# Kernel tuning notes

Measured on AMD Instinct MI355X. Metric: run time of the kernel, lower is better.

The kernel has to match this reference:

```python
import math
import jax, jax.numpy as jnp
import numpy as np

B, C_IN, C_OUT, K, STYLE, H, W = 16, 512, 512, 3, 512, 64, 64


def setup_inputs() -> dict:
    key = jax.random.key(0)
    k1, k2, k3, k4 = jax.random.split(key, 4)
    return {
        "x": jax.random.normal(k1, (B, C_IN, H, W), jnp.float32),
        "style": jax.random.normal(k2, (B, STYLE), jnp.float32),
        "weight": jax.random.normal(k3, (C_OUT, C_IN, K, K), jnp.float32),  # learned conv weight (leading 1 dim of torch param squeezed)
        "mod_w": jax.random.normal(k4, (C_IN, STYLE), jnp.float32),         # EqualLinear weight
        "mod_b": jnp.ones((C_IN,), jnp.float32),                             # EqualLinear bias (bias_init=1)
    }


def reference(x, style, weight, mod_w, mod_b):
    # EqualLinear modulation: scale = 1/sqrt(style_dim), lr_mul = 1
    mod_scale = 1.0 / math.sqrt(STYLE)
    s = style @ (mod_w.T * mod_scale) + mod_b            # [B, C_IN]

    # per-sample modulated weight
    w_scale = 1.0 / math.sqrt(C_IN * K * K)
    w = w_scale * weight[None] * s[:, None, :, None, None]  # [B, C_OUT, C_IN, K, K]

    # demodulate
    demod = jax.lax.rsqrt(jnp.sum(w * w, axis=(2, 3, 4)) + 1e-8)  # [B, C_OUT]
    w = w * demod[:, :, None, None, None]

    pad = K // 2

    def conv_one(xi, wi):
        # xi: [C_IN, H, W], wi: [C_OUT, C_IN, K, K]
        return jax.lax.conv_general_dilated(
            xi[None], wi, window_strides=(1, 1),
            padding=[(pad, pad), (pad, pad)],
            dimension_numbers=("NCHW", "OIHW", "NCHW"),
        )[0]

    return jax.vmap(conv_one)(x, w)  # [B, C_OUT, H, W]
```

## Files before the change

### kernel.cpp

```cpp
#include <hip/hip_runtime.h>
#include <hip/hip_bf16.h>
#include <math.h>
#include <stdint.h>

#define B_     16
#define CI_    512
#define CO_    512
#define HH     64
#define WW     64
#define STYLE_ 512

typedef __bf16 bf16x8 __attribute__((ext_vector_type(8)));
typedef float f32x16 __attribute__((ext_vector_type(16)));

__device__ __forceinline__ int fsl(int r, int h) {
    return (2 * r + (h ^ ((r >> 2) & 1))) ^ (((r >> 4) & 1) << 1);
}

#define WS_S     0
#define WS_DEMOD 32768
#define WS_WSQ   65536
#define WS_WB    1114112
#define WS_XS    5832704

__device__ __forceinline__ void gload16(const void* g, void* l) {
    __builtin_amdgcn_global_load_lds((const __attribute__((address_space(1))) uint32_t*)g,
                                     (__attribute__((address_space(3))) uint32_t*)l, 16, 0, 0);
}

__global__ __launch_bounds__(256) void k_style2(const float* __restrict__ style,
                                                const float* __restrict__ mod_w,
                                                const float* __restrict__ mod_b,
                                                float* __restrict__ s_out) {
    const int ci   = blockIdx.x * 4 + (threadIdx.x >> 6);
    const int b    = blockIdx.y;
    const int lane = threadIdx.x & 63;
    const float4* mw = (const float4*)(mod_w + (size_t)ci * STYLE_);
    const float4* st = (const float4*)(style + (size_t)b * STYLE_);
    float acc = 0.f;
    #pragma unroll
    for (int i = 0; i < 2; ++i) {
        float4 a = mw[lane + i * 64], s = st[lane + i * 64];
        acc += a.x * s.x + a.y * s.y + a.z * s.z + a.w * s.w;
    }
    #pragma unroll
    for (int off = 32; off >= 1; off >>= 1) acc += __shfl_xor(acc, off);
    if (lane == 0)
        s_out[b * CI_ + ci] = acc * 0.044194173824159216f + mod_b[ci];
}

__global__ __launch_bounds__(256) void k_wprep(const float* __restrict__ weight,
                                               float* __restrict__ wsq, __bf16* __restrict__ wb) {
    int p = blockIdx.x * 256 + threadIdx.x;
    int co = p >> 9, ci = p & 511;
    const float* wp = weight + (size_t)p * 9;
    const int sl = fsl(co & 127, (ci >> 3) & 1);
    const int gs = ((co >> 7) << 8) + sl;
    float acc = 0.f;
    #pragma unroll
    for (int t = 0; t < 9; ++t) {
        float v = wp[t];
        acc += v * v;
        wb[(((size_t)(ci >> 4) * 9 + t) * 8192) + gs * 8 + (ci & 7)] = (__bf16)v;
    }
    wsq[(size_t)ci * CO_ + co] = acc;
}

__global__ void k_demod(const float* __restrict__ s, const float* __restrict__ wsq,
                        float* __restrict__ demod) {
    int b = blockIdx.x, co = threadIdx.x;
    const float w_scale2 = 1.0f / 4608.0f;
    float acc = 0.f;
    const float* sb = s + b * CI_;
    for (int ci = 0; ci < CI_; ++ci) { float sv = sb[ci]; acc += sv * sv * wsq[(size_t)ci * CO_ + co]; }
    demod[b * CO_ + co] = 1.0f / sqrtf(acc * w_scale2 + 1e-8f);
}

__global__ __launch_bounds__(256) void k_xs(const float* __restrict__ x, const float* __restrict__ s,
                                            __bf16* __restrict__ xs) {
    __shared__ float Lt[64][65];
    const int y = blockIdx.x, b = blockIdx.y;
    const int tid = threadIdx.x;
    const float w_scale = 0.014731391274719739f;
    for (int ci0 = 0; ci0 < CI_; ci0 += 64) {
        for (int i = tid; i < 64 * 16; i += 256) {
            int ci = i >> 4, x4 = (i & 15) * 4;
            const float4 v = *(const float4*)&x[((size_t)(b * CI_ + ci0 + ci) * HH + y) * WW + x4];
            float sc = s[b * CI_ + ci0 + ci] * w_scale;
            Lt[ci][x4]     = v.x * sc;
            Lt[ci][x4 + 1] = v.y * sc;
            Lt[ci][x4 + 2] = v.z * sc;
            Lt[ci][x4 + 3] = v.w * sc;
        }
        __syncthreads();
        for (int o = tid; o < 512; o += 256) {
            int xx = o >> 3, oct = o & 7;
            int cb = ci0 + oct * 8;
            int chunk = cb >> 4;
            int pp = fsl(xx + 1, oct & 1) - 2;
            bf16x8 v;
            #pragma unroll
            for (int j = 0; j < 8; ++j) v[j] = (__bf16)Lt[oct * 8 + j][xx];
            size_t idx = (((size_t)chunk * 16 + b) * 66 + (y + 1)) * 1024 + pp * 8;
            *(bf16x8*)&xs[idx] = v;
        }
        __syncthreads();
    }
    if (y == 0 || y == 63) {
        const int row = (y == 0) ? 0 : 65;
        uint32_t* xs32 = (uint32_t*)xs;
        for (int c = 0; c < 32; ++c)
            for (int i = tid; i < 512; i += 256)
                xs32[(((size_t)c * 16 + b) * 66 + row) * 512 + i] = 0;
    }
}

#define XBUF 25600
#define WBUF 36864

__global__ __launch_bounds__(512, 1) void k_conv(
    const __bf16* __restrict__ xs, const __bf16* __restrict__ wb,
    const float* __restrict__ demod, float* __restrict__ out)
{
    __shared__ __align__(512) char smem[2 * XBUF + 2 * WBUF];

    const int tid  = threadIdx.x;
    const int lane = tid & 63;
    const int wave = tid >> 6;

    const int bid  = blockIdx.x;
    const int r8   = bid & 7;
    const int q    = bid >> 3;
    const int co0  = (q & 3) * 128;
    const int yb   = (q >> 2) | (r8 << 4);
    const int y0   = (yb & 7) * 8;
    const int b    = yb >> 3;

    const int lm = lane & 31;
    const int g2 = lane >> 5;

    if (tid < 320) {
        int buf = tid / 160, rem = tid % 160;
        int rb = rem >> 4, hh = rem & 15;
        int side = hh >> 3, dw = hh & 7;
        ((uint32_t*)smem)[buf * (XBUF / 4) + rb * 640 + side * 520 + dw] = 0;
    }
    asm volatile("s_waitcnt lgkmcnt(0)" ::: "memory");

    uint32_t soff[9];
    uint32_t sdst[9];
    if (wave < 4) {
        #pragma unroll
        for (int i = 0; i < 5; ++i) {
            int j = wave * 5 + i, rb = j >> 1, seg = j & 1;
            soff[i] = (uint32_t)((y0 + rb) * 1024 + seg * 512 + lane * 8);
            sdst[i] = (uint32_t)(rb * 2560 + 32 + seg * 1024 + lane * 16);
        }
    } else {
        #pragma unroll
        for (int i = 0; i < 9; ++i) {
            int j = (wave - 4) * 9 + i;
            int tap = j >> 2, seg = j & 3;
            soff[i] = (uint32_t)(tap * 8192 + co0 * 16 + seg * 512 + lane * 8);
            sdst[i] = (uint32_t)(j * 1024 + lane * 16);
        }
    }

    const uint32_t abase = (uint32_t)(16 * fsl(lm, g2));
    uint32_t bbase[9];
    #pragma unroll
    for (int kh = 0; kh < 3; ++kh)
        #pragma unroll
        for (int kw = 0; kw < 3; ++kw)
            bbase[kh * 3 + kw] = (uint32_t)((wave + kh) * 2560 + 16 * fsl(lm + kw, g2));

    f32x16 acc[4][2];
    #pragma unroll
    for (int mi = 0; mi < 4; ++mi)
        #pragma unroll
        for (int nt = 0; nt < 2; ++nt)
            #pragma unroll
            for (int r = 0; r < 16; ++r) acc[mi][nt][r] = 0.f;

    auto stage = [&](int chunk, int sel) {
        if (wave < 4) {
            const __bf16* base = xs + (size_t)chunk * 1081344 + (size_t)b * 67584;
            #pragma unroll
            for (int i = 0; i < 5; ++i) gload16(base + soff[i], smem + sel * XBUF + sdst[i]);
        } else {
            const __bf16* base = wb + (size_t)chunk * 73728;
            #pragma unroll
            for (int i = 0; i < 9; ++i) gload16(base + soff[i], smem + 2 * XBUF + sel * WBUF + sdst[i]);
        }
    };

    stage(0, 0);

    for (int t = 0; t < 32; ++t) {
        if (t < 31) {
            stage(t + 1, (t + 1) & 1);
            if (wave < 4) asm volatile("s_waitcnt vmcnt(5)" ::: "memory");
            else          asm volatile("s_waitcnt vmcnt(9)" ::: "memory");
        } else {
            asm volatile("s_waitcnt vmcnt(0)" ::: "memory");
        }
        __builtin_amdgcn_s_barrier();

        const char* xbuf = smem + (t & 1) * XBUF;
        const char* wbuf = smem + 2 * XBUF + (t & 1) * WBUF + abase;

        bf16x8 fa[2][4];
        bf16x8 fb[2][2];
        #pragma unroll
        for (int mi = 0; mi < 4; ++mi) fa[0][mi] = *(const bf16x8*)(wbuf + mi * 1024);
        #pragma unroll
        for (int nt = 0; nt < 2; ++nt) fb[0][nt] = *(const bf16x8*)(xbuf + bbase[0] + nt * 1024);

        __builtin_amdgcn_s_setprio(1);
        #pragma unroll
        for (int tp = 0; tp < 9; ++tp) {
            const int cur = tp & 1, nxt = cur ^ 1;
            if (tp < 8) {
                const char* wp = wbuf + (tp + 1) * 4096;
                #pragma unroll
                for (int mi = 0; mi < 4; ++mi) fa[nxt][mi] = *(const bf16x8*)(wp + mi * 1024);
                #pragma unroll
                for (int nt = 0; nt < 2; ++nt) fb[nxt][nt] = *(const bf16x8*)(xbuf + bbase[tp + 1] + nt * 1024);
            }
            __builtin_amdgcn_sched_barrier(0);
            #pragma unroll
            for (int nt = 0; nt < 2; ++nt) {
                acc[0][nt] = __builtin_amdgcn_mfma_f32_32x32x16_bf16(fa[cur][0], fb[cur][nt], acc[0][nt], 0, 0, 0);
                acc[1][nt] = __builtin_amdgcn_mfma_f32_32x32x16_bf16(fa[cur][1], fb[cur][nt], acc[1][nt], 0, 0, 0);
                acc[2][nt] = __builtin_amdgcn_mfma_f32_32x32x16_bf16(fa[cur][2], fb[cur][nt], acc[2][nt], 0, 0, 0);
                acc[3][nt] = __builtin_amdgcn_mfma_f32_32x32x16_bf16(fa[cur][3], fb[cur][nt], acc[3][nt], 0, 0, 0);
            }
            __builtin_amdgcn_sched_barrier(0);
        }
        __builtin_amdgcn_s_setprio(0);
        __builtin_amdgcn_s_barrier();
    }

    const int y = y0 + wave;
    float* outb = out + (size_t)b * CO_ * 4096 + (size_t)y * 64;
    #pragma unroll
    for (int mi = 0; mi < 4; ++mi) {
        #pragma unroll
        for (int reg = 0; reg < 16; ++reg) {
            const int co = co0 + mi * 32 + (reg & 3) + 8 * (reg >> 2) + 4 * g2;
            const float dm = demod[b * CO_ + co];
            outb[(size_t)co * 4096 + lm]      = acc[mi][0][reg] * dm;
            outb[(size_t)co * 4096 + 32 + lm] = acc[mi][1][reg] * dm;
        }
    }
}

extern "C" void kernel_launch(void* const* d_in, const int* in_sizes, int n_in,
                              void* d_out, int out_size, void* d_ws, size_t ws_size,
                              hipStream_t stream) {
    const float* x      = (const float*)d_in[0];
    const float* style  = (const float*)d_in[1];
    const float* weight = (const float*)d_in[2];
    const float* mod_w  = (const float*)d_in[3];
    const float* mod_b  = (const float*)d_in[4];
    float* out = (float*)d_out;

    char* wsb = (char*)d_ws;
    float*  s_buf = (float*)(wsb + WS_S);
    float*  demod = (float*)(wsb + WS_DEMOD);
    float*  wsq   = (float*)(wsb + WS_WSQ);
    __bf16* wb    = (__bf16*)(wsb + WS_WB);
    __bf16* xs    = (__bf16*)(wsb + WS_XS);

    k_style2<<<dim3(CI_ / 4, B_), dim3(256), 0, stream>>>(style, mod_w, mod_b, s_buf);
    k_wprep<<<dim3(CO_ * CI_ / 256), dim3(256), 0, stream>>>(weight, wsq, wb);
    k_demod<<<dim3(B_), dim3(CO_), 0, stream>>>(s_buf, wsq, demod);
    k_xs<<<dim3(HH, B_), dim3(256), 0, stream>>>(x, s_buf, xs);
    k_conv<<<dim3(512), dim3(512), 0, stream>>>(xs, wb, demod, out);
}
```

Measured before the change: 328.7 us.

## Retile conv to 64-channel blocks with 4 waves and cross-row input reuse

The conv kernel is retiled from 128 output channels x 8 rows per 512-thread block to 64 output channels x 8 rows per 256-thread block, with two blocks per CU and 1024 blocks in total. Each wave now computes two output rows and reuses the loaded input rows across the three kh taps. It loads 4 input-row fragments per kw instead of reloading per tap, which cuts LDS reads per MFMA. The weight prep layout and the LDS row stride change to match. The cost is more global weight traffic per output, because each block covers fewer channels, and the software pipelining of fragment loads across taps is dropped.

New measurement: 319.7 us. -2.7%, faster.

```diff
diff --git a/kernel.cpp b/kernel.cpp
--- a/kernel.cpp
+++ b/kernel.cpp
@@ -54,8 +54,7 @@
     int p = blockIdx.x * 256 + threadIdx.x;
     int co = p >> 9, ci = p & 511;
     const float* wp = weight + (size_t)p * 9;
-    const int sl = fsl(co & 127, (ci >> 3) & 1);
-    const int gs = ((co >> 7) << 8) + sl;
+    const int gs = ((co >> 6) << 7) + fsl(co & 63, (ci >> 3) & 1);
     float acc = 0.f;
     #pragma unroll
     for (int t = 0; t < 9; ++t) {
@@ -115,14 +114,14 @@
     }
 }
 
-#define XBUF 25600
-#define WBUF 36864
-
-__global__ __launch_bounds__(512, 1) void k_conv(
+#define XBUF 21120
+#define WBUF 18432
+
+__global__ __launch_bounds__(256, 2) void k_conv(
     const __bf16* __restrict__ xs, const __bf16* __restrict__ wb,
     const float* __restrict__ demod, float* __restrict__ out)
 {
-    __shared__ __align__(512) char smem[2 * XBUF + 2 * WBUF];
+    __shared__ __align__(128) char smem[2 * XBUF + 2 * WBUF];
 
     const int tid  = threadIdx.x;
     const int lane = tid & 63;
@@ -131,62 +130,63 @@
     const int bid  = blockIdx.x;
     const int r8   = bid & 7;
     const int q    = bid >> 3;
-    const int co0  = (q & 3) * 128;
-    const int yb   = (q >> 2) | (r8 << 4);
-    const int y0   = (yb & 7) * 8;
-    const int b    = yb >> 3;
+    const int co0  = (q & 7) * 64;
+    const int tt   = q >> 3;
+    const int y0   = (tt & 7) * 8;
+    const int b    = r8 * 2 + (tt >> 3);
 
     const int lm = lane & 31;
     const int g2 = lane >> 5;
 
-    if (tid < 320) {
-        int buf = tid / 160, rem = tid % 160;
+    for (int i = tid; i < 320; i += 256) {
+        int buf = i / 160, rem = i % 160;
         int rb = rem >> 4, hh = rem & 15;
         int side = hh >> 3, dw = hh & 7;
-        ((uint32_t*)smem)[buf * (XBUF / 4) + rb * 640 + side * 520 + dw] = 0;
+        ((uint32_t*)smem)[buf * (XBUF / 4) + rb * 528 + side * 520 + dw] = 0;
     }
     asm volatile("s_waitcnt lgkmcnt(0)" ::: "memory");
 
-    uint32_t soff[9];
-    uint32_t sdst[9];
-    if (wave < 4) {
-        #pragma unroll
-        for (int i = 0; i < 5; ++i) {
-            int j = wave * 5 + i, rb = j >> 1, seg = j & 1;
+    uint32_t soff[10];
+    uint32_t sdst[10];
+    if (wave < 2) {
+        #pragma unroll
+        for (int i = 0; i < 10; ++i) {
+            int j = wave * 10 + i, rb = j >> 1, seg = j & 1;
             soff[i] = (uint32_t)((y0 + rb) * 1024 + seg * 512 + lane * 8);
-            sdst[i] = (uint32_t)(rb * 2560 + 32 + seg * 1024 + lane * 16);
+            sdst[i] = (uint32_t)(rb * 2112 + 32 + seg * 1024 + lane * 16);
         }
     } else {
         #pragma unroll
         for (int i = 0; i < 9; ++i) {
-            int j = (wave - 4) * 9 + i;
-            int tap = j >> 2, seg = j & 3;
+            int j = (wave - 2) * 9 + i;
+            int tap = j >> 1, seg = j & 1;
             soff[i] = (uint32_t)(tap * 8192 + co0 * 16 + seg * 512 + lane * 8);
             sdst[i] = (uint32_t)(j * 1024 + lane * 16);
         }
-    }
-
-    const uint32_t abase = (uint32_t)(16 * fsl(lm, g2));
-    uint32_t bbase[9];
-    #pragma unroll
-    for (int kh = 0; kh < 3; ++kh)
-        #pragma unroll
-        for (int kw = 0; kw < 3; ++kw)
-            bbase[kh * 3 + kw] = (uint32_t)((wave + kh) * 2560 + 16 * fsl(lm + kw, g2));
-
-    f32x16 acc[4][2];
-    #pragma unroll
-    for (int mi = 0; mi < 4; ++mi)
-        #pragma unroll
-        for (int nt = 0; nt < 2; ++nt)
-            #pragma unroll
-            for (int r = 0; r < 16; ++r) acc[mi][nt][r] = 0.f;
+        soff[9] = 0; sdst[9] = 0;
+    }
+
+    const uint32_t acol = (uint32_t)(16 * fsl(lm, g2));
+    uint32_t cbase[3];
+    #pragma unroll
+    for (int kw = 0; kw < 3; ++kw) cbase[kw] = (uint32_t)(16 * fsl(lm + kw, g2));
+    uint32_t rbase[4];
+    #pragma unroll
+    for (int rr = 0; rr < 4; ++rr) rbase[rr] = (uint32_t)((2 * wave + rr) * 2112);
+
+    f32x16 acc[2][4];
+    #pragma unroll
+    for (int mi = 0; mi < 2; ++mi)
+        #pragma unroll
+        for (int n = 0; n < 4; ++n)
+            #pragma unroll
+            for (int r = 0; r < 16; ++r) acc[mi][n][r] = 0.f;
 
     auto stage = [&](int chunk, int sel) {
-        if (wave < 4) {
+        if (wave < 2) {
             const __bf16* base = xs + (size_t)chunk * 1081344 + (size_t)b * 67584;
             #pragma unroll
-            for (int i = 0; i < 5; ++i) gload16(base + soff[i], smem + sel * XBUF + sdst[i]);
+            for (int i = 0; i < 10; ++i) gload16(base + soff[i], smem + sel * XBUF + sdst[i]);
         } else {
             const __bf16* base = wb + (size_t)chunk * 73728;
             #pragma unroll
@@ -199,58 +199,60 @@
     for (int t = 0; t < 32; ++t) {
         if (t < 31) {
             stage(t + 1, (t + 1) & 1);
-            if (wave < 4) asm volatile("s_waitcnt vmcnt(5)" ::: "memory");
-            else          asm volatile("s_waitcnt vmcnt(9)" ::: "memory");
+            if (wave < 2) asm volatile("s_waitcnt vmcnt(10)" ::: "memory");
+            else          asm volatile("s_waitcnt vmcnt(9)"  ::: "memory");
         } else {
             asm volatile("s_waitcnt vmcnt(0)" ::: "memory");
         }
         __builtin_amdgcn_s_barrier();
 
         const char* xbuf = smem + (t & 1) * XBUF;
-        const char* wbuf = smem + 2 * XBUF + (t & 1) * WBUF + abase;
-
-        bf16x8 fa[2][4];
-        bf16x8 fb[2][2];
-        #pragma unroll
-        for (int mi = 0; mi < 4; ++mi) fa[0][mi] = *(const bf16x8*)(wbuf + mi * 1024);
-        #pragma unroll
-        for (int nt = 0; nt < 2; ++nt) fb[0][nt] = *(const bf16x8*)(xbuf + bbase[0] + nt * 1024);
+        const char* wbuf = smem + 2 * XBUF + (t & 1) * WBUF + acol;
 
         __builtin_amdgcn_s_setprio(1);
         #pragma unroll
-        for (int tp = 0; tp < 9; ++tp) {
-            const int cur = tp & 1, nxt = cur ^ 1;
-            if (tp < 8) {
-                const char* wp = wbuf + (tp + 1) * 4096;
+        for (int kw = 0; kw < 3; ++kw) {
+            bf16x8 fa[3][2], fb[4][2];
+            #pragma unroll
+            for (int kh = 0; kh < 3; ++kh) {
+                const char* wp = wbuf + (kh * 3 + kw) * 2048;
+                fa[kh][0] = *(const bf16x8*)(wp);
+                fa[kh][1] = *(const bf16x8*)(wp + 1024);
+            }
+            #pragma unroll
+            for (int rr = 0; rr < 4; ++rr) {
+                fb[rr][0] = *(const bf16x8*)(xbuf + rbase[rr] + cbase[kw]);
+                fb[rr][1] = *(const bf16x8*)(xbuf + rbase[rr] + cbase[kw] + 1024);
+            }
+            #pragma unroll
+            for (int kh = 0; kh < 3; ++kh)
                 #pragma unroll
-                for (int mi = 0; mi < 4; ++mi) fa[nxt][mi] = *(const bf16x8*)(wp + mi * 1024);
-                #pragma unroll
-                for (int nt = 0; nt < 2; ++nt) fb[nxt][nt] = *(const bf16x8*)(xbuf + bbase[tp + 1] + nt * 1024);
-            }
-            __builtin_amdgcn_sched_barrier(0);
-            #pragma unroll
-            for (int nt = 0; nt < 2; ++nt) {
-                acc[0][nt] = __builtin_amdgcn_mfma_f32_32x32x16_bf16(fa[cur][0], fb[cur][nt], acc[0][nt], 0, 0, 0);
-                acc[1][nt] = __builtin_amdgcn_mfma_f32_32x32x16_bf16(fa[cur][1], fb[cur][nt], acc[1][nt], 0, 0, 0);
-                acc[2][nt] = __builtin_amdgcn_mfma_f32_32x32x16_bf16(fa[cur][2], fb[cur][nt], acc[2][nt], 0, 0, 0);
-                acc[3][nt] = __builtin_amdgcn_mfma_f32_32x32x16_bf16(fa[cur][3], fb[cur][nt], acc[3][nt], 0, 0, 0);
-            }
-            __builtin_amdgcn_sched_barrier(0);
+                for (int ys = 0; ys < 2; ++ys)
+                    #pragma unroll
+                    for (int nt = 0; nt < 2; ++nt) {
+                        acc[0][ys * 2 + nt] = __builtin_amdgcn_mfma_f32_32x32x16_bf16(
+                            fa[kh][0], fb[ys + kh][nt], acc[0][ys * 2 + nt], 0, 0, 0);
+                        acc[1][ys * 2 + nt] = __builtin_amdgcn_mfma_f32_32x32x16_bf16(
+                            fa[kh][1], fb[ys + kh][nt], acc[1][ys * 2 + nt], 0, 0, 0);
+                    }
         }
         __builtin_amdgcn_s_setprio(0);
         __builtin_amdgcn_s_barrier();
     }
 
-    const int y = y0 + wave;
-    float* outb = out + (size_t)b * CO_ * 4096 + (size_t)y * 64;
-    #pragma unroll
-    for (int mi = 0; mi < 4; ++mi) {
-        #pragma unroll
-        for (int reg = 0; reg < 16; ++reg) {
-            const int co = co0 + mi * 32 + (reg & 3) + 8 * (reg >> 2) + 4 * g2;
-            const float dm = demod[b * CO_ + co];
-            outb[(size_t)co * 4096 + lm]      = acc[mi][0][reg] * dm;
-            outb[(size_t)co * 4096 + 32 + lm] = acc[mi][1][reg] * dm;
+    #pragma unroll
+    for (int mi = 0; mi < 2; ++mi) {
+        #pragma unroll
+        for (int ys = 0; ys < 2; ++ys) {
+            const int y = y0 + 2 * wave + ys;
+            float* outb = out + ((size_t)b * CO_ + co0 + mi * 32) * 4096 + (size_t)y * 64;
+            #pragma unroll
+            for (int reg = 0; reg < 16; ++reg) {
+                const int cosub = (reg & 3) + 8 * (reg >> 2) + 4 * g2;
+                const float dm = demod[b * CO_ + co0 + mi * 32 + cosub];
+                outb[(size_t)cosub * 4096 + lm]      = acc[mi][ys * 2 + 0][reg] * dm;
+                outb[(size_t)cosub * 4096 + 32 + lm] = acc[mi][ys * 2 + 1][reg] * dm;
+            }
         }
     }
 }
@@ -276,5 +278,5 @@
     k_wprep<<<dim3(CO_ * CI_ / 256), dim3(256), 0, stream>>>(weight, wsq, wb);
     k_demod<<<dim3(B_), dim3(CO_), 0, stream>>>(s_buf, wsq, demod);
     k_xs<<<dim3(HH, B_), dim3(256), 0, stream>>>(x, s_buf, xs);
-    k_conv<<<dim3(512), dim3(512), 0, stream>>>(xs, wb, demod, out);
-}
+    k_conv<<<dim3(1024), dim3(256), 0, stream>>>(xs, wb, demod, out);
+}
```
